# Kernel optimization log

Hardware: AMD Instinct MI355X
Metric: run time of the kernel (lower is better)

## Reference

```python
import jax, jax.numpy as jnp
import numpy as np

B, T, C = 2, 2048, 2048
N_HEAD, N_KV_HEAD = 16, 4
HEAD_DIM = C // N_HEAD  # 128
HALF = HEAD_DIM // 2    # 64


def _rms_norm(x):
    # F.rms_norm with no weight: x / sqrt(mean(x^2) + eps), eps = dtype eps
    eps = jnp.finfo(x.dtype).eps
    return x * jax.lax.rsqrt(jnp.mean(x * x, axis=-1, keepdims=True) + eps)


def _rope_apply(x, cos, sin):
    # x: [B, H, T, Hs]; cos/sin: [1, 1, T, Hs/2]
    x1, x2 = x[..., :HALF], x[..., HALF:]
    return jnp.concatenate([x1 * cos - x2 * sin, x1 * sin + x2 * cos], axis=-1)


def setup_inputs() -> dict:
    key = jax.random.key(0)
    ks = jax.random.split(key, 8)
    x = jax.random.normal(ks[0], (B, T, C), dtype=jnp.float32)
    # real RoPE tables (base 10000), shape [1,1,T,HALF]
    inv_freq = 1.0 / (10000.0 ** (np.arange(0, HALF, dtype=np.float32) / HALF))
    t = np.arange(T, dtype=np.float32)
    ang = np.einsum('t,f->tf', t, inv_freq)
    cos = jnp.asarray(np.cos(ang))[None, None]
    sin = jnp.asarray(np.sin(ang))[None, None]
    s = 0.02
    Wq = jax.random.normal(ks[1], (C, N_HEAD * HEAD_DIM), dtype=jnp.float32) * s
    Wk = jax.random.normal(ks[2], (C, N_KV_HEAD * HEAD_DIM), dtype=jnp.float32) * s
    Wv = jax.random.normal(ks[3], (C, N_KV_HEAD * HEAD_DIM), dtype=jnp.float32) * s
    Wo = jax.random.normal(ks[4], (C, C), dtype=jnp.float32) * s
    bo = jnp.zeros((C,), dtype=jnp.float32)
    return {"x": x, "cos": cos, "sin": sin, "Wq": Wq, "Wk": Wk, "Wv": Wv, "Wo": Wo, "bo": bo}


def reference(x, cos, sin, Wq, Wk, Wv, Wo, bo):
    Bq, Tq, Cq = x.shape
    G = N_HEAD // N_KV_HEAD
    # QKV projections (GQA, no bias)
    q = (x @ Wq).reshape(Bq, Tq, N_HEAD, HEAD_DIM)
    k = (x @ Wk).reshape(Bq, Tq, N_KV_HEAD, HEAD_DIM)
    v = (x @ Wv).reshape(Bq, Tq, N_KV_HEAD, HEAD_DIM)
    # QK RMSNorm (over head_dim), then to [B, H, T, Hs]
    q = jnp.transpose(_rms_norm(q), (0, 2, 1, 3))
    k = jnp.transpose(_rms_norm(k), (0, 2, 1, 3))
    v = jnp.transpose(v, (0, 2, 1, 3))
    # RoPE
    q = _rope_apply(q, cos[:, :, :Tq, :], sin[:, :, :Tq, :])
    k = _rope_apply(k, cos[:, :, :Tq, :], sin[:, :, :Tq, :])
    # GQA: repeat kv heads across groups
    k = jnp.repeat(k, G, axis=1)  # [B, H, T, Hs]
    v = jnp.repeat(v, G, axis=1)
    # Causal SDPA
    scale = 1.0 / jnp.sqrt(jnp.asarray(HEAD_DIM, dtype=x.dtype))
    scores = jnp.einsum('bhqd,bhkd->bhqk', q, k) * scale
    causal = jnp.tril(jnp.ones((Tq, Tq), dtype=bool))
    scores = jnp.where(causal, scores, jnp.asarray(-jnp.inf, dtype=scores.dtype))
    attn = jax.nn.softmax(scores, axis=-1)
    y = jnp.einsum('bhqk,bhkd->bhqd', attn, v)
    y = jnp.transpose(y, (0, 2, 1, 3)).reshape(Bq, Tq, Cq)
    return y @ Wo + bo
```

## Files before the change

kernel.cpp:

```cpp
#include <hip/hip_runtime.h>
#include <hip/hip_bf16.h>
#include <math.h>

#define BB 2
#define TT 2048
#define CC 2048
#define NH 16
#define NKV 4
#define HD 128
#define HALF 64
#define MTOT (BB*TT)
#define NQKV (CC + 2*NKV*HD)

typedef unsigned short u16;
typedef __attribute__((ext_vector_type(8))) short bf16x8;
typedef __attribute__((ext_vector_type(4))) float f32x4;

__device__ __forceinline__ u16 f2bf(float f) {
  unsigned u = __float_as_uint(f);
  unsigned r = (u + 0x7FFFu + ((u >> 16) & 1u)) >> 16;
  return (u16)r;
}
__device__ __forceinline__ float bf2f(u16 v) {
  return __uint_as_float(((unsigned)v) << 16);
}

__device__ __forceinline__ void gl_lds16(const void* g, void* l) {
  __builtin_amdgcn_global_load_lds(
      (const __attribute__((address_space(1))) unsigned int*)g,
      (__attribute__((address_space(3))) unsigned int*)l, 16, 0, 0);
}

__global__ __launch_bounds__(256) void prep(
    const float* __restrict__ x, const float* __restrict__ Wq,
    const float* __restrict__ Wk, const float* __restrict__ Wv,
    const float* __restrict__ Wo, u16* __restrict__ xb,
    u16* __restrict__ Wt, u16* __restrict__ Wot) {
  const int z = blockIdx.z;
  const int tx = threadIdx.x, ty = threadIdx.y;
  if (z == 4) {
    const int tid = ty * 32 + tx;
    const int i = (blockIdx.y * 64 + blockIdx.x) * 256 + tid;
    const float4* s4 = (const float4*)x;
    float4 a = s4[(size_t)i * 2], b = s4[(size_t)i * 2 + 1];
    bf16x8 o;
    o[0] = (short)f2bf(a.x); o[1] = (short)f2bf(a.y);
    o[2] = (short)f2bf(a.z); o[3] = (short)f2bf(a.w);
    o[4] = (short)f2bf(b.x); o[5] = (short)f2bf(b.y);
    o[6] = (short)f2bf(b.z); o[7] = (short)f2bf(b.w);
    ((bf16x8*)xb)[i] = o;
    return;
  }
  const float* W; u16* dst; int N; int row_off;
  if (z == 0)      { W = Wq; dst = Wt;  N = 2048; row_off = 0; }
  else if (z == 1) { W = Wk; dst = Wt;  N = 512;  row_off = 2048; }
  else if (z == 2) { W = Wv; dst = Wt;  N = 512;  row_off = 2560; }
  else             { W = Wo; dst = Wot; N = 2048; row_off = 0; }
  const int n0 = blockIdx.x * 32, k0 = blockIdx.y * 32;
  if (n0 >= N) return;
  __shared__ float tile[32][33];
#pragma unroll
  for (int i = 0; i < 4; ++i)
    tile[ty + 8 * i][tx] = W[(size_t)(k0 + ty + 8 * i) * N + n0 + tx];
  __syncthreads();
#pragma unroll
  for (int i = 0; i < 4; ++i)
    dst[(size_t)(row_off + n0 + ty + 8 * i) * CC + k0 + tx] =
        f2bf(tile[tx][ty + 8 * i]);
}

__global__ __launch_bounds__(512, 2) void gemm_8ph(
    const u16* __restrict__ A, const u16* __restrict__ Bt,
    const float* __restrict__ bias, float* __restrict__ C,
    int M, int N, int K, int out_bf16) {
  __shared__ u16 As[32768];
  __shared__ u16 Bs[32768];
  const int tid = threadIdx.x;
  const int w = tid >> 6, lane = tid & 63;
  const int quad = lane >> 4, lo = lane & 15;
  const int wm = w >> 2, wn = w & 3;
  const int bm = blockIdx.y * 256, bn = blockIdx.x * 256;
  const int NT = K >> 6;

  const u16* agp[2][2]; const u16* bgp[2][2];
#pragma unroll
  for (int h = 0; h < 2; ++h)
#pragma unroll
    for (int j = 0; j < 2; ++j) {
      const unsigned X = (unsigned)h * 16384u +
                         (unsigned)((w * 2 + j) * 64 + lane) * 16u;
      const int row = (int)(X >> 7);
      const int ce = (int)(((X & 127u) ^ (((X >> 7) & 7u) << 4)) >> 1);
      agp[h][j] = A  + (size_t)(bm + row) * K + ce;
      bgp[h][j] = Bt + (size_t)(bn + row) * K + ce;
    }
  char* const lAs = (char*)As;
  char* const lBs = (char*)Bs;
  const int woff = w * 2048;

#define STGA(hh, bufp, kt) do { \
    gl_lds16(agp[hh][0] + (size_t)(kt) * 64, lAs + (bufp) * 32768 + (hh) * 16384 + woff); \
    gl_lds16(agp[hh][1] + (size_t)(kt) * 64, lAs + (bufp) * 32768 + (hh) * 16384 + woff + 1024); \
  } while (0)
#define STGB(hh, bufp, kt) do { \
    gl_lds16(bgp[hh][0] + (size_t)(kt) * 64, lBs + (bufp) * 32768 + (hh) * 16384 + woff); \
    gl_lds16(bgp[hh][1] + (size_t)(kt) * 64, lBs + (bufp) * 32768 + (hh) * 16384 + woff + 1024); \
  } while (0)

  const int sw  = (lo & 7) << 4;
  const int co0 = (quad * 16) ^ sw;
  const int co1 = (64 + quad * 16) ^ sw;
  const int aRB = (wm * 128 + lo) * 128;
  const int bRB = (wn * 64 + lo) * 128;

  f32x4 acc[8][4];
#pragma unroll
  for (int ri = 0; ri < 8; ++ri)
#pragma unroll
    for (int ci = 0; ci < 4; ++ci)
#pragma unroll
      for (int r = 0; r < 4; ++r) acc[ri][ci][r] = 0.f;

  STGA(0, 0, 0); STGA(1, 0, 0); STGB(0, 0, 0); STGB(1, 0, 0);
  STGB(0, 1, 1); STGB(1, 1, 1); STGA(0, 1, 1);
  asm volatile("s_waitcnt vmcnt(6)" ::: "memory");
  __builtin_amdgcn_s_barrier();

  for (int t = 0; t < NT; ++t) {
    const int pa = t & 1;
    const char* Ab = lAs + pa * 32768 + aRB;
    const char* Bb = lBs + pa * 32768 + bRB;
    bf16x8 a[4][2], b0[2][2], b1[2][2];

#pragma unroll
    for (int i = 0; i < 4; ++i) {
      a[i][0] = *(const bf16x8*)(Ab + i * 2048 + co0);
      a[i][1] = *(const bf16x8*)(Ab + i * 2048 + co1);
    }
#pragma unroll
    for (int j = 0; j < 2; ++j) {
      b0[j][0] = *(const bf16x8*)(Bb + j * 2048 + co0);
      b0[j][1] = *(const bf16x8*)(Bb + j * 2048 + co1);
    }
    if (t + 1 < NT) STGA(1, (t + 1) & 1, t + 1);
    __builtin_amdgcn_s_barrier();
    asm volatile("s_waitcnt lgkmcnt(0)");
    __builtin_amdgcn_s_setprio(1);
#pragma unroll
    for (int i = 0; i < 4; ++i)
#pragma unroll
      for (int j = 0; j < 2; ++j) {
        acc[i][j] = __builtin_amdgcn_mfma_f32_16x16x32_bf16(a[i][0], b0[j][0], acc[i][j], 0, 0, 0);
        acc[i][j] = __builtin_amdgcn_mfma_f32_16x16x32_bf16(a[i][1], b0[j][1], acc[i][j], 0, 0, 0);
      }
    __builtin_amdgcn_s_setprio(0);
    __builtin_amdgcn_s_barrier();

#pragma unroll
    for (int j = 0; j < 2; ++j) {
      b1[j][0] = *(const bf16x8*)(Bb + 4096 + j * 2048 + co0);
      b1[j][1] = *(const bf16x8*)(Bb + 4096 + j * 2048 + co1);
    }
    __builtin_amdgcn_s_barrier();
    asm volatile("s_waitcnt lgkmcnt(0)");
    __builtin_amdgcn_s_setprio(1);
#pragma unroll
    for (int i = 0; i < 4; ++i)
#pragma unroll
      for (int j = 0; j < 2; ++j) {
        acc[i][2 + j] = __builtin_amdgcn_mfma_f32_16x16x32_bf16(a[i][0], b1[j][0], acc[i][2 + j], 0, 0, 0);
        acc[i][2 + j] = __builtin_amdgcn_mfma_f32_16x16x32_bf16(a[i][1], b1[j][1], acc[i][2 + j], 0, 0, 0);
      }
    __builtin_amdgcn_s_setprio(0);
    __builtin_amdgcn_s_barrier();

#pragma unroll
    for (int i = 0; i < 4; ++i) {
      a[i][0] = *(const bf16x8*)(Ab + 8192 + i * 2048 + co0);
      a[i][1] = *(const bf16x8*)(Ab + 8192 + i * 2048 + co1);
    }
    if (t + 2 < NT) STGB(0, pa, t + 2);
    __builtin_amdgcn_s_barrier();
    asm volatile("s_waitcnt lgkmcnt(0)");
    __builtin_amdgcn_s_setprio(1);
#pragma unroll
    for (int i = 0; i < 4; ++i)
#pragma unroll
      for (int j = 0; j < 2; ++j) {
        acc[4 + i][2 + j] = __builtin_amdgcn_mfma_f32_16x16x32_bf16(a[i][0], b1[j][0], acc[4 + i][2 + j], 0, 0, 0);
        acc[4 + i][2 + j] = __builtin_amdgcn_mfma_f32_16x16x32_bf16(a[i][1], b1[j][1], acc[4 + i][2 + j], 0, 0, 0);
      }
    __builtin_amdgcn_s_setprio(0);
    __builtin_amdgcn_s_barrier();

    if (t + 2 < NT) { STGB(1, pa, t + 2); STGA(0, pa, t + 2); }
    if (t + 2 < NT)      asm volatile("s_waitcnt vmcnt(6)" ::: "memory");
    else if (t + 1 < NT) asm volatile("s_waitcnt vmcnt(0)" ::: "memory");
    __builtin_amdgcn_s_barrier();
    asm volatile("s_waitcnt lgkmcnt(0)");
    __builtin_amdgcn_s_setprio(1);
#pragma unroll
    for (int i = 0; i < 4; ++i)
#pragma unroll
      for (int j = 0; j < 2; ++j) {
        acc[4 + i][j] = __builtin_amdgcn_mfma_f32_16x16x32_bf16(a[i][0], b0[j][0], acc[4 + i][j], 0, 0, 0);
        acc[4 + i][j] = __builtin_amdgcn_mfma_f32_16x16x32_bf16(a[i][1], b0[j][1], acc[4 + i][j], 0, 0, 0);
      }
    __builtin_amdgcn_s_setprio(0);
    __builtin_amdgcn_s_barrier();
  }
#undef STGA
#undef STGB

  const int rbase = bm + wm * 128;
  const int cbase = bn + wn * 64;
#pragma unroll
  for (int ri = 0; ri < 8; ++ri)
#pragma unroll
    for (int ci = 0; ci < 4; ++ci) {
      const int col = cbase + ci * 16 + lo;
      const float bv = bias ? bias[col] : 0.f;
#pragma unroll
      for (int r = 0; r < 4; ++r) {
        const int row = rbase + ri * 16 + quad * 4 + r;
        const float v = acc[ri][ci][r] + bv;
        if (out_bf16) ((u16*)C)[(size_t)row * N + col] = f2bf(v);
        else          C[(size_t)row * N + col] = v;
      }
    }
}

__global__ __launch_bounds__(512, 2) void gemm_n128(
    const u16* __restrict__ A, const u16* __restrict__ Bt,
    const float* __restrict__ bias, float* __restrict__ C,
    int M, int N, int K, int out_bf16) {
  __shared__ u16 As[32768];
  __shared__ u16 Bs[16384];
  const int tid = threadIdx.x;
  const int w = tid >> 6, lane = tid & 63;
  const int quad = lane >> 4, lo = lane & 15;
  const int wm = w >> 1, wn = w & 1;
  const int bm = blockIdx.y * 256, bn = blockIdx.x * 128;
  const int NT = K >> 6;

  const u16* agp[2][2];
#pragma unroll
  for (int h = 0; h < 2; ++h)
#pragma unroll
    for (int j = 0; j < 2; ++j) {
      const unsigned X = (unsigned)h * 16384u +
                         (unsigned)((w * 2 + j) * 64 + lane) * 16u;
      const int row = (int)(X >> 7);
      const int ce = (int)(((X & 127u) ^ (((X >> 7) & 7u) << 4)) >> 1);
      agp[h][j] = A + (size_t)(bm + row) * K + ce;
    }
  const u16* bgp[2];
#pragma unroll
  for (int j = 0; j < 2; ++j) {
    const unsigned X = (unsigned)((w * 2 + j) * 64 + lane) * 16u;
    const int row = (int)(X >> 7);
    const int ce = (int)(((X & 127u) ^ (((X >> 7) & 7u) << 4)) >> 1);
    bgp[j] = Bt + (size_t)(bn + row) * K + ce;
  }
  char* const lAs = (char*)As;
  char* const lBs = (char*)Bs;
  const int woff = w * 2048;

#define STGA_(hh, bufp, kt) do { \
    gl_lds16(agp[hh][0] + (size_t)(kt) * 64, lAs + (bufp) * 32768 + (hh) * 16384 + woff); \
    gl_lds16(agp[hh][1] + (size_t)(kt) * 64, lAs + (bufp) * 32768 + (hh) * 16384 + woff + 1024); \
  } while (0)
#define STGB_(bufp, kt) do { \
    gl_lds16(bgp[0] + (size_t)(kt) * 64, lBs + (bufp) * 16384 + woff); \
    gl_lds16(bgp[1] + (size_t)(kt) * 64, lBs + (bufp) * 16384 + woff + 1024); \
  } while (0)

  const int sw  = (lo & 7) << 4;
  const int co0 = (quad * 16) ^ sw;
  const int co1 = (64 + quad * 16) ^ sw;
  const int aRB = (wm * 64 + lo) * 128;
  const int bRB = (wn * 64 + lo) * 128;

  f32x4 acc[4][4];
#pragma unroll
  for (int i = 0; i < 4; ++i)
#pragma unroll
    for (int ci = 0; ci < 4; ++ci)
#pragma unroll
      for (int r = 0; r < 4; ++r) acc[i][ci][r] = 0.f;

  STGA_(0, 0, 0); STGA_(1, 0, 0); STGB_(0, 0);
  STGB_(1, 1); STGA_(0, 1, 1);
  asm volatile("s_waitcnt vmcnt(4)" ::: "memory");
  __builtin_amdgcn_s_barrier();

  for (int t = 0; t < NT; ++t) {
    const int pa = t & 1;
    const char* Ab = lAs + pa * 32768 + aRB;
    const char* Bb = lBs + pa * 16384 + bRB;
    bf16x8 a[4][2], b[4][2];
#pragma unroll
    for (int i = 0; i < 4; ++i) {
      a[i][0] = *(const bf16x8*)(Ab + i * 2048 + co0);
      a[i][1] = *(const bf16x8*)(Ab + i * 2048 + co1);
    }
#pragma unroll
    for (int ci = 0; ci < 4; ++ci) {
      b[ci][0] = *(const bf16x8*)(Bb + ci * 2048 + co0);
      b[ci][1] = *(const bf16x8*)(Bb + ci * 2048 + co1);
    }
    if (t + 1 < NT) STGA_(1, (t + 1) & 1, t + 1);
    asm volatile("s_waitcnt lgkmcnt(0)");
    __builtin_amdgcn_s_barrier();
    __builtin_amdgcn_s_setprio(1);
#pragma unroll
    for (int i = 0; i < 4; ++i)
#pragma unroll
      for (int ci = 0; ci < 2; ++ci) {
        acc[i][ci] = __builtin_amdgcn_mfma_f32_16x16x32_bf16(a[i][0], b[ci][0], acc[i][ci], 0, 0, 0);
        acc[i][ci] = __builtin_amdgcn_mfma_f32_16x16x32_bf16(a[i][1], b[ci][1], acc[i][ci], 0, 0, 0);
      }
    __builtin_amdgcn_s_setprio(0);
    if (t + 2 < NT) { STGB_(pa, t + 2); STGA_(0, pa, t + 2); }
    if (t + 2 < NT)      asm volatile("s_waitcnt vmcnt(4)" ::: "memory");
    else if (t + 1 < NT) asm volatile("s_waitcnt vmcnt(0)" ::: "memory");
    __builtin_amdgcn_s_setprio(1);
#pragma unroll
    for (int i = 0; i < 4; ++i)
#pragma unroll
      for (int ci = 2; ci < 4; ++ci) {
        acc[i][ci] = __builtin_amdgcn_mfma_f32_16x16x32_bf16(a[i][0], b[ci][0], acc[i][ci], 0, 0, 0);
        acc[i][ci] = __builtin_amdgcn_mfma_f32_16x16x32_bf16(a[i][1], b[ci][1], acc[i][ci], 0, 0, 0);
      }
    __builtin_amdgcn_s_setprio(0);
    __builtin_amdgcn_s_barrier();
  }
#undef STGA_
#undef STGB_

  const int rbase = bm + wm * 64;
  const int cbase = bn + wn * 64;
#pragma unroll
  for (int i = 0; i < 4; ++i)
#pragma unroll
    for (int ci = 0; ci < 4; ++ci) {
      const int col = cbase + ci * 16 + lo;
      const float bv = bias ? bias[col] : 0.f;
#pragma unroll
      for (int r = 0; r < 4; ++r) {
        const int row = rbase + i * 16 + quad * 4 + r;
        const float v = acc[i][ci][r] + bv;
        if (out_bf16) ((u16*)C)[(size_t)row * N + col] = f2bf(v);
        else          C[(size_t)row * N + col] = v;
      }
    }
}

__global__ __launch_bounds__(256) void qkv_post(
    const u16* __restrict__ qkv_lin, const float* __restrict__ cosp,
    const float* __restrict__ sinp, u16* __restrict__ q, u16* __restrict__ k) {
  const int bt = blockIdx.x;
  const int hh = blockIdx.y * 4 + (threadIdx.x >> 6);
  const int lane = threadIdx.x & 63;
  const int t = bt & (TT - 1), b = bt >> 11;
  const int col = (hh < NH) ? hh * HD : CC + (hh - NH) * HD;
  const u16* src = qkv_lin + (size_t)bt * NQKV + col;
  float v1 = bf2f(src[lane]), v2 = bf2f(src[lane + 64]);
  float ss = v1 * v1 + v2 * v2;
#pragma unroll
  for (int mm = 1; mm < 64; mm <<= 1) ss += __shfl_xor(ss, mm, 64);
  float rms = rsqrtf(ss * (1.f / 128.f) + 1.1920929e-7f);
  float c = cosp[t * HALF + lane], s = sinp[t * HALF + lane];
  float o1 = v1 * rms * c - v2 * rms * s;
  float o2 = v1 * rms * s + v2 * rms * c;
  if (hh < NH) {
    u16* dst = q + (((size_t)(b * NH + hh)) * TT + t) * HD;
    dst[lane] = f2bf(o1); dst[lane + 64] = f2bf(o2);
  } else {
    u16* dst = k + (((size_t)(b * NKV + (hh - NH))) * TT + t) * HD;
    dst[lane] = f2bf(o1); dst[lane + 64] = f2bf(o2);
  }
}

__global__ __launch_bounds__(256) void v_transpose(
    const u16* __restrict__ qkv_lin, u16* __restrict__ vt) {
  __shared__ u16 tile[32][33];
  const int t0 = blockIdx.x * 32, d0 = blockIdx.y * 32;
  const int p = blockIdx.z;
  const int b = p >> 2, kv = p & 3;
  const int tx = threadIdx.x, ty = threadIdx.y;
#pragma unroll
  for (int i = 0; i < 4; ++i)
    tile[ty + 8 * i][tx] =
        qkv_lin[(size_t)(b * TT + t0 + ty + 8 * i) * NQKV + CC + NKV * HD + kv * HD + d0 + tx];
  __syncthreads();
  const int tperm = ((tx >> 2) & 3) * 8 + (tx & 3) + 4 * ((tx >> 4) & 1);
#pragma unroll
  for (int i = 0; i < 4; ++i)
    vt[((size_t)p * HD + d0 + ty + 8 * i) * TT + t0 + tperm] = tile[tx][ty + 8 * i];
}

__device__ __forceinline__ void softmax_pack(
    const f32x4* sacc, float& l_lane, bf16x8* ap, int rowq, int t0,
    bool diag, int quad) {
  const float cc = 0.12751744050808612f;
  float e[4][4];
  if (diag) {
#pragma unroll
    for (int ct = 0; ct < 4; ++ct)
#pragma unroll
      for (int r = 0; r < 4; ++r) {
        float v = __builtin_amdgcn_exp2f(sacc[ct][r] * cc);
        if (t0 + ct * 16 + quad * 4 + r > rowq) v = 0.f;
        l_lane += v; e[ct][r] = v;
      }
  } else {
#pragma unroll
    for (int ct = 0; ct < 4; ++ct)
#pragma unroll
      for (int r = 0; r < 4; ++r) {
        float v = __builtin_amdgcn_exp2f(sacc[ct][r] * cc);
        l_lane += v; e[ct][r] = v;
      }
  }
#pragma unroll
  for (int k2 = 0; k2 < 2; ++k2) {
    bf16x8 ch;
#pragma unroll
    for (int j = 0; j < 8; ++j)
      ch[j] = (short)f2bf(e[k2 * 2 + (j >> 2)][j & 3]);
    ap[k2] = ch;
  }
}

__global__ __launch_bounds__(512, 4) void attn_mfma(
    const u16* __restrict__ Qb, const u16* __restrict__ Kb,
    const u16* __restrict__ Vt, u16* __restrict__ Y) {
  __shared__ u16 Ks[2][8192];
  __shared__ u16 Vs[2][8192];

  const int qt = blockIdx.x;
  const int bh = blockIdx.y;
  const int b = bh >> 4, h = bh & 15, kvh = h >> 2;
  const int tid = threadIdx.x;
  const int wave = tid >> 6, lane = tid & 63;
  const int wg = wave >> 2, wv = wave & 3;
  const int quad = lane >> 4, lo = lane & 15;

  const int rows = (wg == 0) ? qt * 64 : (31 - qt) * 64;
  const u16* Qg = Qb + (size_t)(b * NH + h) * TT * HD;
  const u16* Kg = Kb + (size_t)(b * NKV + kvh) * TT * HD;
  const u16* Vg = Vt + (size_t)(b * NKV + kvh) * HD * TT;

  bf16x8 aq[4];
#pragma unroll
  for (int kc = 0; kc < 4; ++kc)
    aq[kc] = *(const bf16x8*)(Qg + (size_t)(rows + wv * 16 + lo) * HD + kc * 32 + quad * 8);

  const u16* kgp[2]; const u16* vgp[2];
  u16* klp[2][2]; u16* vlp[2][2];
#pragma unroll
  for (int c = 0; c < 2; ++c) {
    const int s = wave * 2 + c;
    const int ct = s >> 2, kq = s & 3;
    kgp[c] = Kg + (size_t)(ct * 16 + lo) * HD + kq * 32 + quad * 8;
    const int dt = s >> 1, k2 = s & 1;
    vgp[c] = Vg + (size_t)(dt * 16 + lo) * TT + k2 * 32 + quad * 8;
    klp[0][c] = &Ks[0][s * 512]; klp[1][c] = &Ks[1][s * 512];
    vlp[0][c] = &Vs[0][s * 512]; vlp[1][c] = &Vs[1][s * 512];
  }

  f32x4 oacc[8];
#pragma unroll
  for (int dt = 0; dt < 8; ++dt)
#pragma unroll
    for (int r = 0; r < 4; ++r) oacc[dt][r] = 0.f;
  float l_lane = 0.f;

  const int ntiles = 32 - qt;
  const int rowq = rows + wv * 16 + lo;

#pragma unroll
  for (int c = 0; c < 2; ++c) {
    gl_lds16(kgp[c], klp[0][c]); kgp[c] += 64 * HD;
    gl_lds16(vgp[c], vlp[0][c]); vgp[c] += 64;
  }

  for (int nt = 0; nt < ntiles; ++nt) {
    const int par = nt & 1;
    __syncthreads();
    if (nt + 1 < ntiles) {
#pragma unroll
      for (int c = 0; c < 2; ++c) {
        gl_lds16(kgp[c], klp[par ^ 1][c]); kgp[c] += 64 * HD;
        gl_lds16(vgp[c], vlp[par ^ 1][c]); vgp[c] += 64;
      }
    }
    const bool act = (wg == 1) || (nt <= qt);
    if (act) {
      const u16* ksb = Ks[par];
      const u16* vsb = Vs[par];
      const int t0 = nt * 64;

      f32x4 sacc[4];
#pragma unroll
      for (int ct = 0; ct < 4; ++ct)
#pragma unroll
        for (int r = 0; r < 4; ++r) sacc[ct][r] = 0.f;
      __builtin_amdgcn_s_setprio(1);
#pragma unroll
      for (int ct = 0; ct < 4; ++ct)
#pragma unroll
        for (int kc = 0; kc < 4; ++kc) {
          bf16x8 bk = *(const bf16x8*)&ksb[(ct * 4 + kc) * 512 + lane * 8];
          sacc[ct] = __builtin_amdgcn_mfma_f32_16x16x32_bf16(bk, aq[kc], sacc[ct], 0, 0, 0);
        }
      __builtin_amdgcn_s_setprio(0);

      bf16x8 ap[2];
      softmax_pack(sacc, l_lane, ap, rowq, t0, t0 + 63 > rows + wv * 16, quad);

      __builtin_amdgcn_s_setprio(1);
#pragma unroll
      for (int dt = 0; dt < 8; ++dt)
#pragma unroll
        for (int k2 = 0; k2 < 2; ++k2) {
          bf16x8 bv = *(const bf16x8*)&vsb[(dt * 2 + k2) * 512 + lane * 8];
          oacc[dt] = __builtin_amdgcn_mfma_f32_16x16x32_bf16(ap[k2], bv, oacc[dt], 0, 0, 0);
        }
      __builtin_amdgcn_s_setprio(0);
    }
  }

  float l = l_lane;
  l += __shfl_xor(l, 16, 64);
  l += __shfl_xor(l, 32, 64);
  l = 1.f / l;
  float linv[4];
#pragma unroll
  for (int r = 0; r < 4; ++r)
    linv[r] = __shfl(l, quad * 4 + r, 64);
  const size_t row0 = (size_t)b * TT + rows + wv * 16 + quad * 4;
#pragma unroll
  for (int dt = 0; dt < 8; ++dt)
#pragma unroll
    for (int r = 0; r < 4; ++r)
      Y[(row0 + r) * CC + h * HD + dt * 16 + lo] = f2bf(oacc[dt][r] * linv[r]);
}

extern "C" void kernel_launch(void* const* d_in, const int* in_sizes, int n_in,
                              void* d_out, int out_size, void* d_ws, size_t ws_size,
                              hipStream_t stream) {
  (void)in_sizes; (void)n_in; (void)out_size; (void)ws_size;
  const float* x    = (const float*)d_in[0];
  const float* cosp = (const float*)d_in[1];
  const float* sinp = (const float*)d_in[2];
  const float* Wq   = (const float*)d_in[3];
  const float* Wk   = (const float*)d_in[4];
  const float* Wv   = (const float*)d_in[5];
  const float* Wo   = (const float*)d_in[6];
  const float* bo   = (const float*)d_in[7];
  float* out = (float*)d_out;
  char* ws = (char*)d_ws;

  const size_t MB = 1024 * 1024;
  u16* xb      = (u16*)(ws);
  u16* Wt      = (u16*)(ws + 16 * MB);
  u16* qkv_lin = (u16*)(ws + 28 * MB);
  u16* Wot     = (u16*)(ws + 52 * MB);
  u16* qb_buf  = (u16*)(ws);
  u16* kb      = (u16*)(ws + 16 * MB);
  u16* vt      = (u16*)(ws + 20 * MB);
  u16* y       = (u16*)(ws + 28 * MB);

  prep<<<dim3(64, 64, 5), dim3(32, 8), 0, stream>>>(x, Wq, Wk, Wv, Wo, xb, Wt, Wot);

  gemm_8ph<<<dim3(NQKV / 256, MTOT / 256), 512, 0, stream>>>(
      xb, Wt, nullptr, (float*)qkv_lin, MTOT, NQKV, CC, 1);

  qkv_post<<<dim3(MTOT, 5), 256, 0, stream>>>(qkv_lin, cosp, sinp, qb_buf, kb);

  v_transpose<<<dim3(TT / 32, HD / 32, BB * NKV), dim3(32, 8), 0, stream>>>(qkv_lin, vt);

  attn_mfma<<<dim3(16, BB * NH), 512, 0, stream>>>(qb_buf, kb, vt, y);

  gemm_n128<<<dim3(CC / 128, MTOT / 256), 512, 0, stream>>>(
      y, Wot, bo, out, MTOT, CC, CC, 0);
}
```

Before: 307.0 us.

## Triple-buffer K/V tiles in attention with explicit vmcnt waits

Moves the attention kernel's K/V staging from double to triple buffering in LDS. Loads are now issued two tiles ahead, and each iteration waits with an explicit vmcnt count followed by a raw s_barrier instead of __syncthreads, so more global-load latency can be hidden. It also switches the softmax bf16 packing to the library conversion and relaxes launch bounds to 2 blocks per SM, because LDS use grows to 96KB per block. The trade-off is lower occupancy in exchange for deeper prefetch.

```diff
diff --git a/kernel.cpp b/kernel.cpp
--- a/kernel.cpp
+++ b/kernel.cpp
@@ -20,6 +20,10 @@
   unsigned u = __float_as_uint(f);
   unsigned r = (u + 0x7FFFu + ((u >> 16) & 1u)) >> 16;
   return (u16)r;
+}
+__device__ __forceinline__ u16 f2bf_hw(float f) {
+  __hip_bfloat16 h = __float2bfloat16(f);
+  return *reinterpret_cast<const u16*>(&h);
 }
 __device__ __forceinline__ float bf2f(u16 v) {
   return __uint_as_float(((unsigned)v) << 16);
@@ -428,16 +432,16 @@
     bf16x8 ch;
 #pragma unroll
     for (int j = 0; j < 8; ++j)
-      ch[j] = (short)f2bf(e[k2 * 2 + (j >> 2)][j & 3]);
+      ch[j] = (short)f2bf_hw(e[k2 * 2 + (j >> 2)][j & 3]);
     ap[k2] = ch;
   }
 }
 
-__global__ __launch_bounds__(512, 4) void attn_mfma(
+__global__ __launch_bounds__(512, 2) void attn_mfma(
     const u16* __restrict__ Qb, const u16* __restrict__ Kb,
     const u16* __restrict__ Vt, u16* __restrict__ Y) {
-  __shared__ u16 Ks[2][8192];
-  __shared__ u16 Vs[2][8192];
+  __shared__ u16 Ks[3][8192];
+  __shared__ u16 Vs[3][8192];
 
   const int qt = blockIdx.x;
   const int bh = blockIdx.y;
@@ -458,7 +462,7 @@
     aq[kc] = *(const bf16x8*)(Qg + (size_t)(rows + wv * 16 + lo) * HD + kc * 32 + quad * 8);
 
   const u16* kgp[2]; const u16* vgp[2];
-  u16* klp[2][2]; u16* vlp[2][2];
+  u16* klp[3][2]; u16* vlp[3][2];
 #pragma unroll
   for (int c = 0; c < 2; ++c) {
     const int s = wave * 2 + c;
@@ -466,8 +470,11 @@
     kgp[c] = Kg + (size_t)(ct * 16 + lo) * HD + kq * 32 + quad * 8;
     const int dt = s >> 1, k2 = s & 1;
     vgp[c] = Vg + (size_t)(dt * 16 + lo) * TT + k2 * 32 + quad * 8;
-    klp[0][c] = &Ks[0][s * 512]; klp[1][c] = &Ks[1][s * 512];
-    vlp[0][c] = &Vs[0][s * 512]; vlp[1][c] = &Vs[1][s * 512];
+#pragma unroll
+    for (int p = 0; p < 3; ++p) {
+      klp[p][c] = &Ks[p][s * 512];
+      vlp[p][c] = &Vs[p][s * 512];
+    }
   }
 
   f32x4 oacc[8];
@@ -485,15 +492,23 @@
     gl_lds16(kgp[c], klp[0][c]); kgp[c] += 64 * HD;
     gl_lds16(vgp[c], vlp[0][c]); vgp[c] += 64;
   }
-
+#pragma unroll
+  for (int c = 0; c < 2; ++c) {
+    gl_lds16(kgp[c], klp[1][c]); kgp[c] += 64 * HD;
+    gl_lds16(vgp[c], vlp[1][c]); vgp[c] += 64;
+  }
+
+  int par = 0;
   for (int nt = 0; nt < ntiles; ++nt) {
-    const int par = nt & 1;
-    __syncthreads();
-    if (nt + 1 < ntiles) {
+    if (nt + 1 < ntiles) asm volatile("s_waitcnt vmcnt(4)" ::: "memory");
+    else                 asm volatile("s_waitcnt vmcnt(0)" ::: "memory");
+    __builtin_amdgcn_s_barrier();
+    if (nt + 2 < ntiles) {
+      const int ps = (nt + 2 < 3) ? (nt + 2) : (nt + 2) % 3;
 #pragma unroll
       for (int c = 0; c < 2; ++c) {
-        gl_lds16(kgp[c], klp[par ^ 1][c]); kgp[c] += 64 * HD;
-        gl_lds16(vgp[c], vlp[par ^ 1][c]); vgp[c] += 64;
+        gl_lds16(kgp[c], klp[ps][c]); kgp[c] += 64 * HD;
+        gl_lds16(vgp[c], vlp[ps][c]); vgp[c] += 64;
       }
     }
     const bool act = (wg == 1) || (nt <= qt);
@@ -530,6 +545,7 @@
         }
       __builtin_amdgcn_s_setprio(0);
     }
+    par = (par == 2) ? 0 : par + 1;
   }
 
   float l = l_lane;
```

Result: slower. 365.9 us (+19.2%).
